# Kernel tuning notes

Measured on AMD Instinct MI355X. Metric: run time of the kernel, lower is better.

## Reference

```python
import jax, jax.numpy as jnp
import numpy as np

NEG = 1.0e12  # large subtractive penalty from the original code


def setup_inputs() -> dict:
    key = jax.random.key(0)
    k1, k2, k3, k4 = jax.random.split(key, 4)
    b, q_len, ns, ls, e = 8, 512, 64, 128, 256
    q = jax.random.normal(k1, (b, q_len, e), dtype=jnp.float32)
    k = jax.random.normal(k2, (b, ns, ls, e), dtype=jnp.float32)
    v = jax.random.normal(k3, (b, ns, ls, e), dtype=jnp.float32)
    mask = jax.random.randint(k4, (b, ns, ls), 0, 2) > 0  # bool, True = keep
    return {"q": q, "k": k, "v": v, "mask": mask}


def reference(q, k, v, mask):
    # scores: (b, q_len, num_snippet, len_snippet)
    attn = jnp.einsum("bqe,bsle->bqsl", q, k)
    # original: attn = attn - (~mask) * 1e12, broadcast over q_len
    penalty = jnp.where(mask, 0.0, NEG).astype(attn.dtype)  # (b, s, l)
    attn = attn - penalty[:, None, :, :]
    attn = jax.nn.softmax(attn, axis=3)  # softmax within each snippet
    # weighted sum over len_snippet -> (b, q_len, num_snippet, e_dim)
    out = jnp.einsum("bqsl,bsle->bqse", attn, v)
    return out
```

## Files before the change

kernel.cpp:

```cpp
#include <hip/hip_runtime.h>

typedef _Float16 half8  __attribute__((ext_vector_type(8)));
typedef _Float16 half2v __attribute__((ext_vector_type(2)));
typedef float    f32x4  __attribute__((ext_vector_type(4)));
typedef float    f32x2  __attribute__((ext_vector_type(2)));

#define QLEN  512
#define NS    64
#define LS    128
#define EDIM  256
#define QT    64

#define KLOAD(dst, lt) do {                                                   \
  _Pragma("unroll") for (int it = 0; it < 4; ++it) {                          \
    int f = it * 2048 + tid * 8; int r = f >> 8; int e0 = f & 255;            \
    const float* src = kbase + (size_t)((lt) * 32 + r) * EDIM + e0;           \
    dst[2*it]   = *(const f32x4*)src;                                         \
    dst[2*it+1] = *(const f32x4*)(src + 4); } } while (0)

#define KSTORE(sv, bi) do {                                                   \
  _Pragma("unroll") for (int it = 0; it < 4; ++it) {                          \
    int f = it * 2048 + tid * 8; int r = f >> 8; int e0 = f & 255;            \
    f32x4 a = sv[2*it], d = sv[2*it+1]; half8 h;                              \
    h[0]=(_Float16)a[0]; h[1]=(_Float16)a[1]; h[2]=(_Float16)a[2]; h[3]=(_Float16)a[3]; \
    h[4]=(_Float16)d[0]; h[5]=(_Float16)d[1]; h[6]=(_Float16)d[2]; h[7]=(_Float16)d[3]; \
    *(half8*)(kvbuf + (bi) * 16384 + r * 512 + ((e0 * 2) ^ ((r & 7) << 4))) = h; } } while (0)

#define VLOAD(d, lt) do {                                                     \
  _Pragma("unroll") for (int jj = 0; jj < 2; ++jj)                            \
  _Pragma("unroll") for (int j = 0; j < 8; ++j) {                             \
    int l = (lt) * 32 + vlh * 16 + jj * 8 + j;                                \
    d[jj*8+j] = *(const f32x2*)(vbase + (size_t)l * EDIM + 2 * vp); } } while (0)

#define VSTORE(sv, lt) do {                                                   \
  _Pragma("unroll") for (int jj = 0; jj < 2; ++jj) {                          \
    half8 h0, h1;                                                             \
    _Pragma("unroll") for (int j = 0; j < 8; ++j) {                           \
      h0[j] = (_Float16)sv[jj*8+j][0]; h1[j] = (_Float16)sv[jj*8+j][1]; }     \
    int l0 = (((lt) & 1) * 32 + vlh * 16 + jj * 8) * 2;                       \
    int sw = (vp & 7) << 4;                                                   \
    *(half8*)(kvbuf + (2*vp    ) * 128 + (l0 ^ sw)) = h0;                     \
    *(half8*)(kvbuf + (2*vp + 1) * 128 + (l0 ^ sw)) = h1; } } while (0)

#define PV(lt) do {                                                           \
  half8 af = *(const half8*)(pw + c * 256 + ((((lt) * 64) + g * 16) ^ (c << 4))); \
  _Pragma("unroll") for (int et = 0; et < 16; ++et) {                         \
    int e = et * 16 + c;                                                      \
    half8 bf = *(const half8*)(kvbuf + e * 128 +                              \
                 (((((lt) & 1) * 64) + g * 16) ^ (((e >> 1) & 7) << 4)));     \
    oacc[et] = __builtin_amdgcn_mfma_f32_16x16x32_f16(af, bf, oacc[et], 0, 0, 0); } } while (0)

__global__ __launch_bounds__(256, 3)
void DotAttn_20083267076209_kernel(const float* __restrict__ qg,
                                   const float* __restrict__ kg,
                                   const float* __restrict__ vg,
                                   const int*   __restrict__ maskg,
                                   float*       __restrict__ outg)
{
    __shared__ __align__(16) unsigned char kvbuf[32768];
    __shared__ __align__(16) unsigned char pbuf[4][4096];

    const int tid  = threadIdx.x;
    const int w    = tid >> 6;
    const int lane = tid & 63;
    const int c    = lane & 15;
    const int g    = lane >> 4;
    const int vp   = tid & 127;
    const int vlh  = tid >> 7;

    const int bid = blockIdx.x;
    const int xcd = bid & 7;
    const int qt  = (bid >> 3) & 7;
    const int b   = (bid >> 6) & 7;
    const int s   = (bid >> 9) * 8 + xcd;

    const float* kbase = kg + (size_t)(b * NS + s) * LS * EDIM;
    const float* vbase = vg + (size_t)(b * NS + s) * LS * EDIM;
    const float* qbase = qg + ((size_t)b * QLEN + (size_t)qt * QT + (size_t)w * 16) * EDIM;
    unsigned char* pw  = pbuf[w];

    int mbits = 0;
    {
        const int* mb = maskg + (b * NS + s) * LS;
#pragma unroll
        for (int t = 0; t < 8; ++t)
            if (mb[t * 16 + c] != 0) mbits |= (1 << t);
    }

    half8 qf[8];
#pragma unroll
    for (int ks = 0; ks < 8; ++ks) {
        const float* p = qbase + (size_t)c * EDIM + ks * 32 + g * 8;
        f32x4 a = *(const f32x4*)p;
        f32x4 d = *(const f32x4*)(p + 4);
        half8 h;
        h[0]=(_Float16)a[0]; h[1]=(_Float16)a[1]; h[2]=(_Float16)a[2]; h[3]=(_Float16)a[3];
        h[4]=(_Float16)d[0]; h[5]=(_Float16)d[1]; h[6]=(_Float16)d[2]; h[7]=(_Float16)d[3];
        qf[ks] = h;
    }

    f32x4 kr[8];
    f32x2 vrA[16], vrB[16];
    KLOAD(kr, 0);

    f32x4 sacc[8];
#pragma unroll
    for (int t = 0; t < 8; ++t) sacc[t] = (f32x4){0.f, 0.f, 0.f, 0.f};

#pragma unroll
    for (int lt = 0; lt < 4; ++lt) {
        KSTORE(kr, lt & 1);
        if (lt < 3) KLOAD(kr, lt + 1);
        else        VLOAD(vrA, 0);
        __syncthreads();
        const unsigned char* kb = kvbuf + (lt & 1) * 16384;
#pragma unroll
        for (int lb = 0; lb < 2; ++lb) {
            int row  = lb * 16 + c;
            int base = row * 512;
            int sw   = (c & 7) << 4;
#pragma unroll
            for (int ks = 0; ks < 8; ++ks) {
                half8 bf = *(const half8*)(kb + base + ((ks * 64 + g * 16) ^ sw));
                sacc[lt * 2 + lb] =
                    __builtin_amdgcn_mfma_f32_16x16x32_f16(qf[ks], bf, sacc[lt * 2 + lb], 0, 0, 0);
            }
        }
    }

#pragma unroll
    for (int t = 0; t < 8; ++t)
        if (!((mbits >> t) & 1)) {
            sacc[t][0] = -1e30f; sacc[t][1] = -1e30f;
            sacc[t][2] = -1e30f; sacc[t][3] = -1e30f;
        }
#pragma unroll
    for (int r = 0; r < 4; ++r) {
        float m = sacc[0][r];
#pragma unroll
        for (int t = 1; t < 8; ++t) m = fmaxf(m, sacc[t][r]);
        m = fmaxf(m, __shfl_xor(m, 1, 64));
        m = fmaxf(m, __shfl_xor(m, 2, 64));
        m = fmaxf(m, __shfl_xor(m, 4, 64));
        m = fmaxf(m, __shfl_xor(m, 8, 64));
        float sum = 0.f;
#pragma unroll
        for (int t = 0; t < 8; ++t) {
            float pp = __expf(sacc[t][r] - m);
            sacc[t][r] = pp;
            sum += pp;
        }
        sum += __shfl_xor(sum, 1, 64);
        sum += __shfl_xor(sum, 2, 64);
        sum += __shfl_xor(sum, 4, 64);
        sum += __shfl_xor(sum, 8, 64);
        float inv = 1.f / sum;
#pragma unroll
        for (int t = 0; t < 8; ++t) sacc[t][r] *= inv;
    }

#pragma unroll
    for (int t = 0; t < 8; ++t) {
#pragma unroll
        for (int r = 0; r < 4; ++r) {
            float v  = sacc[t][r];
            float vn = __shfl_xor(v, 1, 64);
            if (!(c & 1)) {
                half2v h2; h2[0] = (_Float16)v; h2[1] = (_Float16)vn;
                int q = 4 * g + r;
                *(half2v*)(pw + q * 256 + ((2 * (t * 16 + c)) ^ (q << 4))) = h2;
            }
        }
    }

    VLOAD(vrB, 1);
    __syncthreads();

    f32x4 oacc[16];
#pragma unroll
    for (int et = 0; et < 16; ++et) oacc[et] = (f32x4){0.f, 0.f, 0.f, 0.f};

    VSTORE(vrA, 0);
    VSTORE(vrB, 1);
    VLOAD(vrA, 2);
    VLOAD(vrB, 3);
    __syncthreads();
    PV(0);
    PV(1);
    __syncthreads();
    VSTORE(vrA, 2);
    VSTORE(vrB, 3);
    __syncthreads();
    PV(2);
    PV(3);

    float* ob = outg + (((size_t)b * QLEN + (size_t)qt * QT + w * 16 + 4 * g) * NS + s) * EDIM + c;
#pragma unroll
    for (int et = 0; et < 16; ++et) {
#pragma unroll
        for (int r = 0; r < 4; ++r)
            ob[(size_t)r * NS * EDIM + et * 16] = oacc[et][r];
    }
}

extern "C" void kernel_launch(void* const* d_in, const int* in_sizes, int n_in,
                              void* d_out, int out_size, void* d_ws, size_t ws_size,
                              hipStream_t stream) {
    const float* q    = (const float*)d_in[0];
    const float* k    = (const float*)d_in[1];
    const float* v    = (const float*)d_in[2];
    const int*   mask = (const int*)d_in[3];
    float* out = (float*)d_out;
    dim3 grid(4096);
    dim3 block(256);
    hipLaunchKernelGGL(DotAttn_20083267076209_kernel, grid, block, 0, stream,
                       q, k, v, mask, out);
}
```

Before: 166.6 us.

## Transpose MFMA operands to keep P in registers and vectorize output stores

Swaps the MFMA operand order so the score tiles come out transposed (keys along rows), which lets the softmax reduce across lanes with two shuffles. The probabilities are then packed to fp16 and rearranged with lane shuffles directly into the PV A-operand, removing the per-wave LDS P buffer and its stores and loads. V staging is reworked into a smaller 64-key-wide swizzled double buffer, filled one 32-row tile at a time and interleaved with the PV steps. The output is written as 16-byte vector stores. The mask is read with ballots, and barriers become s_waitcnt plus s_barrier. More barriers in the PV phase and more shuffle work are the trade-off.

```diff
diff --git a/kernel.cpp b/kernel.cpp
--- a/kernel.cpp
+++ b/kernel.cpp
@@ -1,15 +1,20 @@
 #include <hip/hip_runtime.h>
 
 typedef _Float16 half8  __attribute__((ext_vector_type(8)));
-typedef _Float16 half2v __attribute__((ext_vector_type(2)));
 typedef float    f32x4  __attribute__((ext_vector_type(4)));
 typedef float    f32x2  __attribute__((ext_vector_type(2)));
+typedef unsigned int u32;
 
 #define QLEN  512
 #define NS    64
 #define LS    128
 #define EDIM  256
-#define QT    64
+
+__device__ __forceinline__ void block_sync_lds() {
+    asm volatile("s_waitcnt lgkmcnt(0)" ::: "memory");
+    __builtin_amdgcn_s_barrier();
+    asm volatile("" ::: "memory");
+}
 
 #define KLOAD(dst, lt) do {                                                   \
   _Pragma("unroll") for (int it = 0; it < 4; ++it) {                          \
@@ -26,29 +31,40 @@
     h[4]=(_Float16)d[0]; h[5]=(_Float16)d[1]; h[6]=(_Float16)d[2]; h[7]=(_Float16)d[3]; \
     *(half8*)(kvbuf + (bi) * 16384 + r * 512 + ((e0 * 2) ^ ((r & 7) << 4))) = h; } } while (0)
 
-#define VLOAD(d, lt) do {                                                     \
+#define VLOAD(lt) do {                                                        \
   _Pragma("unroll") for (int jj = 0; jj < 2; ++jj)                            \
   _Pragma("unroll") for (int j = 0; j < 8; ++j) {                             \
     int l = (lt) * 32 + vlh * 16 + jj * 8 + j;                                \
-    d[jj*8+j] = *(const f32x2*)(vbase + (size_t)l * EDIM + 2 * vp); } } while (0)
-
-#define VSTORE(sv, lt) do {                                                   \
+    vr[jj*8+j] = *(const f32x2*)(vbase + (size_t)l * EDIM + 2 * vp); } } while (0)
+
+#define VSTORE(lt) do {                                                       \
   _Pragma("unroll") for (int jj = 0; jj < 2; ++jj) {                          \
     half8 h0, h1;                                                             \
     _Pragma("unroll") for (int j = 0; j < 8; ++j) {                           \
-      h0[j] = (_Float16)sv[jj*8+j][0]; h1[j] = (_Float16)sv[jj*8+j][1]; }     \
-    int l0 = (((lt) & 1) * 32 + vlh * 16 + jj * 8) * 2;                       \
-    int sw = (vp & 7) << 4;                                                   \
-    *(half8*)(kvbuf + (2*vp    ) * 128 + (l0 ^ sw)) = h0;                     \
-    *(half8*)(kvbuf + (2*vp + 1) * 128 + (l0 ^ sw)) = h1; } } while (0)
+      h0[j] = (_Float16)vr[jj*8+j][0]; h1[j] = (_Float16)vr[jj*8+j][1]; }     \
+    int l0 = (vlh * 16 + jj * 8) * 2;                                         \
+    int sw = (vp & 3) << 4;                                                   \
+    unsigned char* vb = kvbuf + ((lt) & 1) * 16384;                           \
+    *(half8*)(vb + (2*vp    ) * 64 + (l0 ^ sw)) = h0;                         \
+    *(half8*)(vb + (2*vp + 1) * 64 + (l0 ^ sw)) = h1; } } while (0)
 
 #define PV(lt) do {                                                           \
-  half8 af = *(const half8*)(pw + c * 256 + ((((lt) * 64) + g * 16) ^ (c << 4))); \
+  u32 zx = sel2 ? pk0[2*(lt)+1] : pk0[2*(lt)];                                \
+  u32 zy = sel2 ? pk1[2*(lt)+1] : pk1[2*(lt)];                                \
+  u32 wx = sel2 ? pk0[2*(lt)]   : pk0[2*(lt)+1];                              \
+  u32 wy = sel2 ? pk1[2*(lt)]   : pk1[2*(lt)+1];                              \
+  u32 az0 = (u32)__shfl((int)zx, s0, 64), az1 = (u32)__shfl((int)zy, s0, 64); \
+  u32 aw0 = (u32)__shfl((int)wx, s0, 64), aw1 = (u32)__shfl((int)wy, s0, 64); \
+  u32 bz0 = (u32)__shfl((int)zx, s1, 64), bz1 = (u32)__shfl((int)zy, s1, 64); \
+  u32 bw0 = (u32)__shfl((int)wx, s1, 64), bw1 = (u32)__shfl((int)wy, s1, 64); \
+  union { u32 u[4]; half8 h; } pf;                                            \
+  pf.u[0] = useZ ? az0 : aw0;  pf.u[1] = useZ ? az1 : aw1;                    \
+  pf.u[2] = useZ ? bz0 : bw0;  pf.u[3] = useZ ? bz1 : bw1;                    \
+  const unsigned char* vb = kvbuf + ((lt) & 1) * 16384;                       \
   _Pragma("unroll") for (int et = 0; et < 16; ++et) {                         \
     int e = et * 16 + c;                                                      \
-    half8 bf = *(const half8*)(kvbuf + e * 128 +                              \
-                 (((((lt) & 1) * 64) + g * 16) ^ (((e >> 1) & 7) << 4)));     \
-    oacc[et] = __builtin_amdgcn_mfma_f32_16x16x32_f16(af, bf, oacc[et], 0, 0, 0); } } while (0)
+    half8 vf = *(const half8*)(vb + e * 64 + ((g * 16) ^ (((e >> 1) & 3) << 4))); \
+    oacc[et] = __builtin_amdgcn_mfma_f32_16x16x32_f16(vf, pf.h, oacc[et], 0, 0, 0); } } while (0)
 
 __global__ __launch_bounds__(256, 3)
 void DotAttn_20083267076209_kernel(const float* __restrict__ qg,
@@ -58,16 +74,20 @@
                                    float*       __restrict__ outg)
 {
     __shared__ __align__(16) unsigned char kvbuf[32768];
-    __shared__ __align__(16) unsigned char pbuf[4][4096];
 
     const int tid  = threadIdx.x;
-    const int w    = tid >> 6;
     const int lane = tid & 63;
     const int c    = lane & 15;
     const int g    = lane >> 4;
     const int vp   = tid & 127;
     const int vlh  = tid >> 7;
 
+    const bool sel2 = (g >= 2);
+    const bool useZ = (g == 0) || (g == 3);
+    const int  s0   = c + ((g & 1) << 5);
+    const int  s1   = s0 + 16;
+    const int  w    = tid >> 6;
+
     const int bid = blockIdx.x;
     const int xcd = bid & 7;
     const int qt  = (bid >> 3) & 7;
@@ -76,16 +96,11 @@
 
     const float* kbase = kg + (size_t)(b * NS + s) * LS * EDIM;
     const float* vbase = vg + (size_t)(b * NS + s) * LS * EDIM;
-    const float* qbase = qg + ((size_t)b * QLEN + (size_t)qt * QT + (size_t)w * 16) * EDIM;
-    unsigned char* pw  = pbuf[w];
-
-    int mbits = 0;
-    {
-        const int* mb = maskg + (b * NS + s) * LS;
-#pragma unroll
-        for (int t = 0; t < 8; ++t)
-            if (mb[t * 16 + c] != 0) mbits |= (1 << t);
-    }
+    const float* qbase = qg + ((size_t)b * QLEN + (size_t)qt * 64 + (size_t)w * 16) * EDIM;
+
+    const int* mb = maskg + (b * NS + s) * LS;
+    unsigned long long m0 = __ballot(mb[lane] != 0);
+    unsigned long long m1 = __ballot(mb[64 + lane] != 0);
 
     half8 qf[8];
 #pragma unroll
@@ -100,7 +115,7 @@
     }
 
     f32x4 kr[8];
-    f32x2 vrA[16], vrB[16];
+    f32x2 vr[16];
     KLOAD(kr, 0);
 
     f32x4 sacc[8];
@@ -111,8 +126,8 @@
     for (int lt = 0; lt < 4; ++lt) {
         KSTORE(kr, lt & 1);
         if (lt < 3) KLOAD(kr, lt + 1);
-        else        VLOAD(vrA, 0);
-        __syncthreads();
+        else        VLOAD(0);
+        block_sync_lds();
         const unsigned char* kb = kvbuf + (lt & 1) * 16384;
 #pragma unroll
         for (int lb = 0; lb < 2; ++lb) {
@@ -121,86 +136,78 @@
             int sw   = (c & 7) << 4;
 #pragma unroll
             for (int ks = 0; ks < 8; ++ks) {
-                half8 bf = *(const half8*)(kb + base + ((ks * 64 + g * 16) ^ sw));
+                half8 kf = *(const half8*)(kb + base + ((ks * 64 + g * 16) ^ sw));
                 sacc[lt * 2 + lb] =
-                    __builtin_amdgcn_mfma_f32_16x16x32_f16(qf[ks], bf, sacc[lt * 2 + lb], 0, 0, 0);
+                    __builtin_amdgcn_mfma_f32_16x16x32_f16(kf, qf[ks], sacc[lt * 2 + lb], 0, 0, 0);
             }
         }
     }
 
 #pragma unroll
-    for (int t = 0; t < 8; ++t)
-        if (!((mbits >> t) & 1)) {
-            sacc[t][0] = -1e30f; sacc[t][1] = -1e30f;
-            sacc[t][2] = -1e30f; sacc[t][3] = -1e30f;
-        }
-#pragma unroll
-    for (int r = 0; r < 4; ++r) {
-        float m = sacc[0][r];
-#pragma unroll
-        for (int t = 1; t < 8; ++t) m = fmaxf(m, sacc[t][r]);
-        m = fmaxf(m, __shfl_xor(m, 1, 64));
-        m = fmaxf(m, __shfl_xor(m, 2, 64));
-        m = fmaxf(m, __shfl_xor(m, 4, 64));
-        m = fmaxf(m, __shfl_xor(m, 8, 64));
+    for (int t = 0; t < 8; ++t) {
+        unsigned bits = (unsigned)(((t < 4 ? m0 : m1) >> ((t & 3) * 16 + 4 * g)) & 0xFull);
+#pragma unroll
+        for (int r = 0; r < 4; ++r)
+            if (!((bits >> r) & 1)) sacc[t][r] = -1e30f;
+    }
+
+    {
+        float m = sacc[0][0];
+#pragma unroll
+        for (int t = 0; t < 8; ++t)
+#pragma unroll
+            for (int r = 0; r < 4; ++r) m = fmaxf(m, sacc[t][r]);
+        m = fmaxf(m, __shfl_xor(m, 16, 64));
+        m = fmaxf(m, __shfl_xor(m, 32, 64));
         float sum = 0.f;
 #pragma unroll
-        for (int t = 0; t < 8; ++t) {
-            float pp = __expf(sacc[t][r] - m);
-            sacc[t][r] = pp;
-            sum += pp;
-        }
-        sum += __shfl_xor(sum, 1, 64);
-        sum += __shfl_xor(sum, 2, 64);
-        sum += __shfl_xor(sum, 4, 64);
-        sum += __shfl_xor(sum, 8, 64);
+        for (int t = 0; t < 8; ++t)
+#pragma unroll
+            for (int r = 0; r < 4; ++r) {
+                float p = __expf(sacc[t][r] - m);
+                sacc[t][r] = p;
+                sum += p;
+            }
+        sum += __shfl_xor(sum, 16, 64);
+        sum += __shfl_xor(sum, 32, 64);
         float inv = 1.f / sum;
 #pragma unroll
-        for (int t = 0; t < 8; ++t) sacc[t][r] *= inv;
-    }
-
+        for (int t = 0; t < 8; ++t)
+#pragma unroll
+            for (int r = 0; r < 4; ++r) sacc[t][r] *= inv;
+    }
+
+    u32 pk0[8], pk1[8];
 #pragma unroll
     for (int t = 0; t < 8; ++t) {
-#pragma unroll
-        for (int r = 0; r < 4; ++r) {
-            float v  = sacc[t][r];
-            float vn = __shfl_xor(v, 1, 64);
-            if (!(c & 1)) {
-                half2v h2; h2[0] = (_Float16)v; h2[1] = (_Float16)vn;
-                int q = 4 * g + r;
-                *(half2v*)(pw + q * 256 + ((2 * (t * 16 + c)) ^ (q << 4))) = h2;
-            }
-        }
-    }
-
-    VLOAD(vrB, 1);
-    __syncthreads();
+        pk0[t] = __builtin_bit_cast(u32, __builtin_amdgcn_cvt_pkrtz(sacc[t][0], sacc[t][1]));
+        pk1[t] = __builtin_bit_cast(u32, __builtin_amdgcn_cvt_pkrtz(sacc[t][2], sacc[t][3]));
+    }
 
     f32x4 oacc[16];
 #pragma unroll
     for (int et = 0; et < 16; ++et) oacc[et] = (f32x4){0.f, 0.f, 0.f, 0.f};
 
-    VSTORE(vrA, 0);
-    VSTORE(vrB, 1);
-    VLOAD(vrA, 2);
-    VLOAD(vrB, 3);
-    __syncthreads();
+    VSTORE(0);
+    VLOAD(1);
+    block_sync_lds();
     PV(0);
+    VSTORE(1);
+    VLOAD(2);
+    block_sync_lds();
     PV(1);
-    __syncthreads();
-    VSTORE(vrA, 2);
-    VSTORE(vrB, 3);
-    __syncthreads();
+    VSTORE(2);
+    VLOAD(3);
+    block_sync_lds();
     PV(2);
+    VSTORE(3);
+    block_sync_lds();
     PV(3);
 
-    float* ob = outg + (((size_t)b * QLEN + (size_t)qt * QT + w * 16 + 4 * g) * NS + s) * EDIM + c;
-#pragma unroll
-    for (int et = 0; et < 16; ++et) {
-#pragma unroll
-        for (int r = 0; r < 4; ++r)
-            ob[(size_t)r * NS * EDIM + et * 16] = oacc[et][r];
-    }
+    float* ob = outg + (((size_t)b * QLEN + (size_t)qt * 64 + w * 16 + c) * NS + s) * EDIM + 4 * g;
+#pragma unroll
+    for (int et = 0; et < 16; ++et)
+        *(f32x4*)(ob + et * 16) = oacc[et];
 }
 
 extern "C" void kernel_launch(void* const* d_in, const int* in_sizes, int n_in,
```

After: 169.6 us. Within noise of the previous version (+1.8%).
